# Kernel optimization log

Hardware: AMD Instinct MI355X
Metric: run time of the kernel (lower is better)

The kernel has to match this reference:

```python
import jax, jax.numpy as jnp
import numpy as np

NUM_HEAD = 16
DIM_HEAD = 64
SCALE = DIM_HEAD ** -0.5


def setup_inputs() -> dict:
    key = jax.random.key(0)
    k1, k2, k3 = jax.random.split(key, 3)
    B, N, D = 4, 2048, 1024
    x = jax.random.normal(k1, (B, N, D), dtype=jnp.float32)
    w_qkv = jax.random.normal(k2, (D, 3 * NUM_HEAD * DIM_HEAD), dtype=jnp.float32) * (D ** -0.5)
    w_out = jax.random.normal(k3, (NUM_HEAD * DIM_HEAD, D), dtype=jnp.float32) * ((NUM_HEAD * DIM_HEAD) ** -0.5)
    return {"x": x, "w_qkv": w_qkv, "w_out": w_out}


def reference(x, w_qkv, w_out):
    B, N, D = x.shape
    qkv = x @ w_qkv  # [B, N, 3*H*Dh]
    q, k, v = jnp.split(qkv, 3, axis=-1)
    def heads(t):
        return t.reshape(B, N, NUM_HEAD, DIM_HEAD).transpose(0, 2, 1, 3)  # b h n d
    q, k, v = heads(q), heads(k), heads(v)
    scores = jnp.einsum('bhnd,bhmd->bhnm', q, k) * SCALE
    attn = jax.nn.softmax(scores, axis=-1)
    out = jnp.einsum('bhnm,bhmd->bhnd', attn, v)
    out = out.transpose(0, 2, 1, 3).reshape(B, N, NUM_HEAD * DIM_HEAD)
    return out @ w_out
```

## Files before the change

### kernel.cpp

```cpp
#include <hip/hip_runtime.h>
#include <hip/hip_bf16.h>
#include <stdint.h>


typedef __attribute__((ext_vector_type(8))) __bf16 bf16x8;
typedef __attribute__((ext_vector_type(4))) __bf16 bf16x4;
typedef __attribute__((ext_vector_type(4))) float f32x4;
typedef __attribute__((ext_vector_type(16))) float f32x16;
typedef __attribute__((ext_vector_type(4))) unsigned int u32x4;

#define EXPC 0.18033688011112042f
#define THRR 64.0f

static __device__ __forceinline__ void gload_lds16(const void* g, void* s) {
  __builtin_amdgcn_global_load_lds(
      (__attribute__((address_space(1))) unsigned int*)g,
      (__attribute__((address_space(3))) unsigned int*)s, 16, 0, 0);
}

static __device__ __forceinline__ unsigned pk2(float lo, float hi) {
  unsigned short a = __builtin_bit_cast(unsigned short, (__bf16)lo);
  unsigned short b = __builtin_bit_cast(unsigned short, (__bf16)hi);
  return (unsigned)a | ((unsigned)b << 16);
}

__global__ void k_cvt(const float* __restrict__ src, __bf16* __restrict__ dst, int n4) {
  int i = blockIdx.x * blockDim.x + threadIdx.x;
  if (i >= n4) return;
  float4 v = reinterpret_cast<const float4*>(src)[i];
  bf16x4 o = { (__bf16)v.x, (__bf16)v.y, (__bf16)v.z, (__bf16)v.w };
  *reinterpret_cast<bf16x4*>(dst + (size_t)i * 4) = o;
}

__global__ void k_tcvt(const float* __restrict__ src, __bf16* __restrict__ dst, int W, int Hs) {
  __shared__ float tile[32][33];
  int tx = threadIdx.x, ty = threadIdx.y;
  int x = blockIdx.x * 32 + tx;
  int y0 = blockIdx.y * 32;
  for (int j = ty; j < 32; j += 8) tile[j][tx] = src[(size_t)(y0 + j) * W + x];
  __syncthreads();
  int xo = y0 + tx;
  int yo = blockIdx.x * 32;
  for (int j = ty; j < 32; j += 8) dst[(size_t)(yo + j) * Hs + xo] = (__bf16)tile[tx][j];
}

static __device__ __forceinline__ void gemm_core(
    const __bf16* __restrict__ A, const __bf16* __restrict__ BT, int K,
    int m0, int n0, f32x4 acc[4][4], __bf16* As, __bf16* Bs) {
  const int tid = threadIdx.x;
  const int lane = tid & 63, w = tid >> 6;
  const int fr = lane & 15, fq = lane >> 4;
  const int srow = lane >> 2, scol = (lane & 3) * 8;
  const int wr = (w >> 1) * 64, wc = (w & 1) * 64;
#pragma unroll
  for (int mi = 0; mi < 4; ++mi)
#pragma unroll
    for (int nj = 0; nj < 4; ++nj) acc[mi][nj] = (f32x4){0.f, 0.f, 0.f, 0.f};

  for (int ko = 0; ko < K; ko += 32) {
#pragma unroll
    for (int i = 0; i < 2; ++i) {
      int rb = w * 32 + i * 16;
      gload_lds16(A + (size_t)(m0 + rb + srow) * K + ko + scol, As + rb * 32);
      gload_lds16(BT + (size_t)(n0 + rb + srow) * K + ko + scol, Bs + rb * 32);
    }
    __syncthreads();
    bf16x8 af[4], bfv[4];
#pragma unroll
    for (int mi = 0; mi < 4; ++mi)
      af[mi] = *(const bf16x8*)(As + (wr + mi * 16 + fr) * 32 + fq * 8);
#pragma unroll
    for (int nj = 0; nj < 4; ++nj)
      bfv[nj] = *(const bf16x8*)(Bs + (wc + nj * 16 + fr) * 32 + fq * 8);
#pragma unroll
    for (int mi = 0; mi < 4; ++mi)
#pragma unroll
      for (int nj = 0; nj < 4; ++nj)
        acc[mi][nj] = __builtin_amdgcn_mfma_f32_16x16x32_bf16(af[mi], bfv[nj], acc[mi][nj], 0, 0, 0);
    __syncthreads();
  }
}

__global__ __launch_bounds__(256) void k_gemm_qkv(
    const __bf16* __restrict__ A, const __bf16* __restrict__ BT,
    __bf16* __restrict__ qb, __bf16* __restrict__ kb, __bf16* __restrict__ vb) {
  __shared__ __align__(16) __bf16 As[128 * 32];
  __shared__ __align__(16) __bf16 Bs[128 * 32];
  f32x4 acc[4][4];
  int m0 = blockIdx.x * 128, n0 = blockIdx.y * 128;
  gemm_core(A, BT, 1024, m0, n0, acc, As, Bs);
  const int lane = threadIdx.x & 63, w = threadIdx.x >> 6;
  const int fr = lane & 15, fq = lane >> 4;
  const int wr = (w >> 1) * 64, wc = (w & 1) * 64;
  const int which = n0 >> 10;
#pragma unroll
  for (int mi = 0; mi < 4; ++mi) {
#pragma unroll
    for (int nj = 0; nj < 4; ++nj) {
      int row = m0 + wr + mi * 16 + fq * 4;
      int col = n0 + wc + nj * 16 + fr;
      int rem = col & 1023, h = rem >> 6, d = rem & 63;
      int bb = row >> 11, n = row & 2047;
      int bh = bb * 16 + h;
      if (which == 2) {
        bf16x4 pk = { (__bf16)acc[mi][nj][0], (__bf16)acc[mi][nj][1],
                      (__bf16)acc[mi][nj][2], (__bf16)acc[mi][nj][3] };
        *reinterpret_cast<bf16x4*>(vb + ((size_t)bh * 64 + d) * 2048 + n) = pk;
      } else {
        __bf16* dst = (which == 0) ? qb : kb;
#pragma unroll
        for (int j = 0; j < 4; ++j)
          dst[((size_t)bh * 2048 + (n + j)) * 64 + d] = (__bf16)acc[mi][nj][j];
      }
    }
  }
}

__global__ __launch_bounds__(256) void k_gemm_out(
    const __bf16* __restrict__ A, const __bf16* __restrict__ BT, float* __restrict__ C) {
  __shared__ __align__(16) __bf16 As[128 * 32];
  __shared__ __align__(16) __bf16 Bs[128 * 32];
  f32x4 acc[4][4];
  int m0 = blockIdx.x * 128, n0 = blockIdx.y * 128;
  gemm_core(A, BT, 1024, m0, n0, acc, As, Bs);
  const int lane = threadIdx.x & 63, w = threadIdx.x >> 6;
  const int fr = lane & 15, fq = lane >> 4;
  const int wr = (w >> 1) * 64, wc = (w & 1) * 64;
#pragma unroll
  for (int mi = 0; mi < 4; ++mi)
#pragma unroll
    for (int nj = 0; nj < 4; ++nj)
#pragma unroll
      for (int j = 0; j < 4; ++j)
        C[(size_t)(m0 + wr + mi * 16 + fq * 4 + j) * 1024 + n0 + wc + nj * 16 + fr] =
            acc[mi][nj][j];
}

__global__ __launch_bounds__(256, 3) void k_attn(
    const __bf16* __restrict__ qb, const __bf16* __restrict__ kb,
    const __bf16* __restrict__ vb, __bf16* __restrict__ ao) {
  __shared__ __align__(16) __bf16 Ks[2][64 * 64];
  __shared__ __align__(16) __bf16 Vs[2][64 * 64];
  __shared__ __align__(16) __bf16 Qs[4][32 * 64];
  const int tid = threadIdx.x, lane = tid & 63, wid = tid >> 6;
  const int r31 = lane & 31, hi = lane >> 5;
  const int lsw = (lane & 7) ^ ((lane >> 3) & 3);
  const int bh = blockIdx.x & 63, qblk = blockIdx.x >> 6;
  const __bf16* kbase = kb + (size_t)bh * 2048 * 64;
  const __bf16* vbase = vb + (size_t)bh * 64 * 2048;

  const int nbase = qblk * 128 + wid * 32;

  f32x16 o0, o1;
#pragma unroll
  for (int r = 0; r < 16; ++r) { o0[r] = 0.f; o1[r] = 0.f; }
  float m = -1e30f, lsum = 0.f;

  auto stage = [&](int buf, int j0) {
#pragma unroll
    for (int p2 = 0; p2 < 2; ++p2) {
      int row = p2 * 32 + (tid >> 3);
      int sc = (tid & 7) ^ (row & 7) ^ ((row >> 3) & 3);
      int dst = p2 * 2048 + wid * 512;
      gload_lds16(kbase + (size_t)(j0 + row) * 64 + sc * 8, &Ks[buf][dst]);
      gload_lds16(vbase + (size_t)row * 2048 + j0 + sc * 8, &Vs[buf][dst]);
    }
  };

#pragma unroll
  for (int i = 0; i < 4; ++i) {
    int qr = i * 8 + (lane >> 3);
    int qc = (lane & 7) ^ (qr & 7) ^ ((qr >> 3) & 3);
    gload_lds16(qb + ((size_t)bh * 2048 + nbase + qr) * 64 + qc * 8, &Qs[wid][i * 512]);
  }
  stage(0, 0);
  __syncthreads();

  for (int kt = 0; kt < 32; ++kt) {
    const int cur = kt & 1;
    if (kt < 31) stage(cur ^ 1, (kt + 1) * 64);

    f32x16 sa0, sa1;
#pragma unroll
    for (int r = 0; r < 16; ++r) { sa0[r] = 0.f; sa1[r] = 0.f; }
    __builtin_amdgcn_s_setprio(1);
#pragma unroll
    for (int dd = 0; dd < 4; ++dd) {
      bf16x8 qv = *(const bf16x8*)(&Qs[wid][r31 * 64 + (((dd * 2 + hi) ^ lsw) << 3)]);
      bf16x8 k0 = *(const bf16x8*)(&Ks[cur][r31 * 64 + (((dd * 2 + hi) ^ lsw) << 3)]);
      bf16x8 k1 = *(const bf16x8*)(&Ks[cur][(32 + r31) * 64 + (((dd * 2 + hi) ^ lsw) << 3)]);
      sa0 = __builtin_amdgcn_mfma_f32_32x32x16_bf16(k0, qv, sa0, 0, 0, 0);
      sa1 = __builtin_amdgcn_mfma_f32_32x32x16_bf16(k1, qv, sa1, 0, 0, 0);
    }
    __builtin_amdgcn_s_setprio(0);

    float mx[8];
#pragma unroll
    for (int r = 0; r < 8; ++r)
      mx[r] = fmaxf(fmaxf(fmaxf(sa0[2 * r], sa0[2 * r + 1]), sa1[2 * r]), sa1[2 * r + 1]);
#pragma unroll
    for (int s = 4; s > 0; s >>= 1)
#pragma unroll
      for (int r = 0; r < s; ++r) mx[r] = fmaxf(mx[r], mx[r + s]);
    float pmax = fmaxf(mx[0], __shfl_xor(mx[0], 32, 64));

    if (!__all(pmax - m <= THRR)) {
      float mn = fmaxf(m, pmax);
      float corr = __builtin_amdgcn_exp2f((m - mn) * EXPC);
      m = mn;
      lsum *= corr;
#pragma unroll
      for (int r = 0; r < 16; ++r) {
        int qrow = (r & 3) + 8 * (r >> 2) + 4 * hi;
        float cr = __shfl(corr, qrow, 64);
        o0[r] *= cr; o1[r] *= cr;
      }
    }

    const float mneg = -m * EXPC;
    float rs0 = 0.f, rs1 = 0.f, rs2 = 0.f, rs3 = 0.f;
    unsigned pw0[8], pw1[8];
#pragma unroll
    for (int r = 0; r < 8; ++r) {
      float e0 = __builtin_amdgcn_exp2f(fmaf(sa0[2 * r], EXPC, mneg));
      float e1 = __builtin_amdgcn_exp2f(fmaf(sa0[2 * r + 1], EXPC, mneg));
      float e2 = __builtin_amdgcn_exp2f(fmaf(sa1[2 * r], EXPC, mneg));
      float e3 = __builtin_amdgcn_exp2f(fmaf(sa1[2 * r + 1], EXPC, mneg));
      rs0 += e0; rs1 += e1; rs2 += e2; rs3 += e3;
      pw0[r] = pk2(e0, e1);
      pw1[r] = pk2(e2, e3);
    }
    lsum += (rs0 + rs1) + (rs2 + rs3);

    __builtin_amdgcn_s_setprio(1);
#define PVSTEP(W0, W1, W2, W3, KK) do {                                              \
      unsigned a0 = (W0), a1 = (W1), b0 = (W2), b1 = (W3);                           \
      asm("v_permlane32_swap_b32 %0, %1" : "+v"(a0), "+v"(b0));                      \
      asm("v_permlane32_swap_b32 %0, %1" : "+v"(a1), "+v"(b1));                      \
      u32x4 fw = {a0, a1, b0, b1};                                                   \
      bf16x8 pa = __builtin_bit_cast(bf16x8, fw);                                    \
      bf16x8 v0 = *(const bf16x8*)(&Vs[cur][r31 * 64 + ((((KK)*2 + hi) ^ lsw) << 3)]); \
      bf16x8 v1 = *(const bf16x8*)(&Vs[cur][(32 + r31) * 64 + ((((KK)*2 + hi) ^ lsw) << 3)]); \
      o0 = __builtin_amdgcn_mfma_f32_32x32x16_bf16(pa, v0, o0, 0, 0, 0);             \
      o1 = __builtin_amdgcn_mfma_f32_32x32x16_bf16(pa, v1, o1, 0, 0, 0);             \
    } while (0)
    PVSTEP(pw0[0], pw0[1], pw0[2], pw0[3], 0);
    PVSTEP(pw0[4], pw0[5], pw0[6], pw0[7], 1);
    PVSTEP(pw1[0], pw1[1], pw1[2], pw1[3], 2);
    PVSTEP(pw1[4], pw1[5], pw1[6], pw1[7], 3);
#undef PVSTEP
    __builtin_amdgcn_s_setprio(0);

    __syncthreads();
  }

  lsum += __shfl_xor(lsum, 32, 64);
  float inv = 1.0f / lsum;
  const int b = bh >> 4, h = bh & 15;
  __bf16* abase = ao + ((size_t)b * 2048 + nbase) * 1024 + h * 64 + r31;
#pragma unroll
  for (int r = 0; r < 16; ++r) {
    int qrow = (r & 3) + 8 * (r >> 2) + 4 * hi;
    float ir = __shfl(inv, qrow, 64);
    abase[(size_t)qrow * 1024] = (__bf16)(o0[r] * ir);
    abase[(size_t)qrow * 1024 + 32] = (__bf16)(o1[r] * ir);
  }
}

extern "C" void kernel_launch(void* const* d_in, const int* in_sizes, int n_in,
                              void* d_out, int out_size, void* d_ws, size_t ws_size,
                              hipStream_t stream) {
  (void)in_sizes; (void)n_in; (void)out_size; (void)ws_size;
  const float* x = (const float*)d_in[0];
  const float* w_qkv = (const float*)d_in[1];
  const float* w_out = (const float*)d_in[2];
  float* out = (float*)d_out;

  char* p = (char*)d_ws;
  __bf16* xb    = (__bf16*)p; p += (size_t)8192 * 1024 * 2;
  __bf16* wqkvT = (__bf16*)p; p += (size_t)3072 * 1024 * 2;
  __bf16* woutT = (__bf16*)p; p += (size_t)1024 * 1024 * 2;
  __bf16* qb    = (__bf16*)p; p += (size_t)64 * 2048 * 64 * 2;
  __bf16* kb    = (__bf16*)p; p += (size_t)64 * 2048 * 64 * 2;
  __bf16* vb    = (__bf16*)p; p += (size_t)64 * 64 * 2048 * 2;
  __bf16* ao    = (__bf16*)p; p += (size_t)8192 * 1024 * 2;

  k_cvt<<<8192, 256, 0, stream>>>(x, xb, 2097152);
  k_tcvt<<<dim3(96, 32), dim3(32, 8), 0, stream>>>(w_qkv, wqkvT, 3072, 1024);
  k_tcvt<<<dim3(32, 32), dim3(32, 8), 0, stream>>>(w_out, woutT, 1024, 1024);
  k_gemm_qkv<<<dim3(64, 24), 256, 0, stream>>>(xb, wqkvT, qb, kb, vb);
  k_attn<<<dim3(1024), dim3(256), 0, stream>>>(qb, kb, vb, ao);
  k_gemm_out<<<dim3(64, 8), 256, 0, stream>>>(ao, woutT, out);
}
```

Measured before the change: 215.8 us.

## Load K/V fragments directly from global memory instead of LDS double-buffering

The attention kernel drops the shared-memory double-buffered K/V staging and the per-iteration block barrier. Each wave now reads its MFMA K and V operands straight from global memory (relying on L1/L2 for reuse across the four waves), and occupancy is raised to 4 blocks per SM. It also swaps the software bf16 packing for the v_cvt_pk_bf16_f32 instruction and shortens the row-sum accumulation. This removes LDS traffic and synchronisation, at the risk of exposing global-load latency with no explicit prefetch and of redundant cache reads across waves.

```diff
diff --git a/kernel.cpp b/kernel.cpp
--- a/kernel.cpp
+++ b/kernel.cpp
@@ -16,12 +16,6 @@
   __builtin_amdgcn_global_load_lds(
       (__attribute__((address_space(1))) unsigned int*)g,
       (__attribute__((address_space(3))) unsigned int*)s, 16, 0, 0);
-}
-
-static __device__ __forceinline__ unsigned pk2(float lo, float hi) {
-  unsigned short a = __builtin_bit_cast(unsigned short, (__bf16)lo);
-  unsigned short b = __builtin_bit_cast(unsigned short, (__bf16)hi);
-  return (unsigned)a | ((unsigned)b << 16);
 }
 
 __global__ void k_cvt(const float* __restrict__ src, __bf16* __restrict__ dst, int n4) {
@@ -136,36 +130,15 @@
             acc[mi][nj][j];
 }
 
-__global__ __launch_bounds__(256, 3) void k_attn(
+__global__ __launch_bounds__(256, 4) void k_attn(
     const __bf16* __restrict__ qb, const __bf16* __restrict__ kb,
     const __bf16* __restrict__ vb, __bf16* __restrict__ ao) {
-  __shared__ __align__(16) __bf16 Ks[2][64 * 64];
-  __shared__ __align__(16) __bf16 Vs[2][64 * 64];
   __shared__ __align__(16) __bf16 Qs[4][32 * 64];
   const int tid = threadIdx.x, lane = tid & 63, wid = tid >> 6;
   const int r31 = lane & 31, hi = lane >> 5;
   const int lsw = (lane & 7) ^ ((lane >> 3) & 3);
   const int bh = blockIdx.x & 63, qblk = blockIdx.x >> 6;
-  const __bf16* kbase = kb + (size_t)bh * 2048 * 64;
-  const __bf16* vbase = vb + (size_t)bh * 64 * 2048;
-
   const int nbase = qblk * 128 + wid * 32;
-
-  f32x16 o0, o1;
-#pragma unroll
-  for (int r = 0; r < 16; ++r) { o0[r] = 0.f; o1[r] = 0.f; }
-  float m = -1e30f, lsum = 0.f;
-
-  auto stage = [&](int buf, int j0) {
-#pragma unroll
-    for (int p2 = 0; p2 < 2; ++p2) {
-      int row = p2 * 32 + (tid >> 3);
-      int sc = (tid & 7) ^ (row & 7) ^ ((row >> 3) & 3);
-      int dst = p2 * 2048 + wid * 512;
-      gload_lds16(kbase + (size_t)(j0 + row) * 64 + sc * 8, &Ks[buf][dst]);
-      gload_lds16(vbase + (size_t)row * 2048 + j0 + sc * 8, &Vs[buf][dst]);
-    }
-  };
 
 #pragma unroll
   for (int i = 0; i < 4; ++i) {
@@ -173,12 +146,19 @@
     int qc = (lane & 7) ^ (qr & 7) ^ ((qr >> 3) & 3);
     gload_lds16(qb + ((size_t)bh * 2048 + nbase + qr) * 64 + qc * 8, &Qs[wid][i * 512]);
   }
-  stage(0, 0);
-  __syncthreads();
+  asm volatile("s_waitcnt vmcnt(0)" ::: "memory");
+  __builtin_amdgcn_sched_barrier(0);
+
+  const __bf16* kp = kb + (size_t)bh * 2048 * 64 + r31 * 64 + hi * 8;
+  const __bf16* vp = vb + (size_t)bh * 64 * 2048 + r31 * 2048 + hi * 8;
+
+  f32x16 o0, o1;
+#pragma unroll
+  for (int r = 0; r < 16; ++r) { o0[r] = 0.f; o1[r] = 0.f; }
+  float m = -1e30f, lsum = 0.f;
 
   for (int kt = 0; kt < 32; ++kt) {
-    const int cur = kt & 1;
-    if (kt < 31) stage(cur ^ 1, (kt + 1) * 64);
+    const int j0 = kt * 64;
 
     f32x16 sa0, sa1;
 #pragma unroll
@@ -187,8 +167,8 @@
 #pragma unroll
     for (int dd = 0; dd < 4; ++dd) {
       bf16x8 qv = *(const bf16x8*)(&Qs[wid][r31 * 64 + (((dd * 2 + hi) ^ lsw) << 3)]);
-      bf16x8 k0 = *(const bf16x8*)(&Ks[cur][r31 * 64 + (((dd * 2 + hi) ^ lsw) << 3)]);
-      bf16x8 k1 = *(const bf16x8*)(&Ks[cur][(32 + r31) * 64 + (((dd * 2 + hi) ^ lsw) << 3)]);
+      bf16x8 k0 = *(const bf16x8*)(kp + (size_t)j0 * 64 + dd * 16);
+      bf16x8 k1 = *(const bf16x8*)(kp + (size_t)(j0 + 32) * 64 + dd * 16);
       sa0 = __builtin_amdgcn_mfma_f32_32x32x16_bf16(k0, qv, sa0, 0, 0, 0);
       sa1 = __builtin_amdgcn_mfma_f32_32x32x16_bf16(k1, qv, sa1, 0, 0, 0);
     }
@@ -218,7 +198,7 @@
     }
 
     const float mneg = -m * EXPC;
-    float rs0 = 0.f, rs1 = 0.f, rs2 = 0.f, rs3 = 0.f;
+    float rs0 = 0.f, rs1 = 0.f;
     unsigned pw0[8], pw1[8];
 #pragma unroll
     for (int r = 0; r < 8; ++r) {
@@ -226,11 +206,11 @@
       float e1 = __builtin_amdgcn_exp2f(fmaf(sa0[2 * r + 1], EXPC, mneg));
       float e2 = __builtin_amdgcn_exp2f(fmaf(sa1[2 * r], EXPC, mneg));
       float e3 = __builtin_amdgcn_exp2f(fmaf(sa1[2 * r + 1], EXPC, mneg));
-      rs0 += e0; rs1 += e1; rs2 += e2; rs3 += e3;
-      pw0[r] = pk2(e0, e1);
-      pw1[r] = pk2(e2, e3);
-    }
-    lsum += (rs0 + rs1) + (rs2 + rs3);
+      rs0 += e0 + e1; rs1 += e2 + e3;
+      asm("v_cvt_pk_bf16_f32 %0, %1, %2" : "=v"(pw0[r]) : "v"(e0), "v"(e1));
+      asm("v_cvt_pk_bf16_f32 %0, %1, %2" : "=v"(pw1[r]) : "v"(e2), "v"(e3));
+    }
+    lsum += rs0 + rs1;
 
     __builtin_amdgcn_s_setprio(1);
 #define PVSTEP(W0, W1, W2, W3, KK) do {                                              \
@@ -239,8 +219,8 @@
       asm("v_permlane32_swap_b32 %0, %1" : "+v"(a1), "+v"(b1));                      \
       u32x4 fw = {a0, a1, b0, b1};                                                   \
       bf16x8 pa = __builtin_bit_cast(bf16x8, fw);                                    \
-      bf16x8 v0 = *(const bf16x8*)(&Vs[cur][r31 * 64 + ((((KK)*2 + hi) ^ lsw) << 3)]); \
-      bf16x8 v1 = *(const bf16x8*)(&Vs[cur][(32 + r31) * 64 + ((((KK)*2 + hi) ^ lsw) << 3)]); \
+      bf16x8 v0 = *(const bf16x8*)(vp + j0 + (KK) * 16);                             \
+      bf16x8 v1 = *(const bf16x8*)(vp + (size_t)32 * 2048 + j0 + (KK) * 16);         \
       o0 = __builtin_amdgcn_mfma_f32_32x32x16_bf16(pa, v0, o0, 0, 0, 0);             \
       o1 = __builtin_amdgcn_mfma_f32_32x32x16_bf16(pa, v1, o1, 0, 0, 0);             \
     } while (0)
@@ -250,8 +230,6 @@
     PVSTEP(pw1[4], pw1[5], pw1[6], pw1[7], 3);
 #undef PVSTEP
     __builtin_amdgcn_s_setprio(0);
-
-    __syncthreads();
   }
 
   lsum += __shfl_xor(lsum, 32, 64);
```

Result: slower. 336.4 us (+55.9%).

## Keep Q in registers, split KV tile into halves, raise attention occupancy

Applied to the files above, without the earlier changes.

The attention kernel now loads Q fragments straight from global memory into registers instead of staging them through LDS. Each 64-key tile is processed as two 32-key halves with separate softmax updates, which halves the live score registers. Launch bounds move from 3 to 4 blocks per CU, and the bf16 packing uses the v_cvt_pk_bf16_f32 instruction. The aim is higher occupancy and less LDS traffic, at the cost of more online-softmax max/rescale steps and shorter MFMA chains per half.

```diff
diff --git a/kernel.cpp b/kernel.cpp
--- a/kernel.cpp
+++ b/kernel.cpp
@@ -16,12 +16,6 @@
   __builtin_amdgcn_global_load_lds(
       (__attribute__((address_space(1))) unsigned int*)g,
       (__attribute__((address_space(3))) unsigned int*)s, 16, 0, 0);
-}
-
-static __device__ __forceinline__ unsigned pk2(float lo, float hi) {
-  unsigned short a = __builtin_bit_cast(unsigned short, (__bf16)lo);
-  unsigned short b = __builtin_bit_cast(unsigned short, (__bf16)hi);
-  return (unsigned)a | ((unsigned)b << 16);
 }
 
 __global__ void k_cvt(const float* __restrict__ src, __bf16* __restrict__ dst, int n4) {
@@ -136,12 +130,11 @@
             acc[mi][nj][j];
 }
 
-__global__ __launch_bounds__(256, 3) void k_attn(
+__global__ __launch_bounds__(256, 4) void k_attn(
     const __bf16* __restrict__ qb, const __bf16* __restrict__ kb,
     const __bf16* __restrict__ vb, __bf16* __restrict__ ao) {
   __shared__ __align__(16) __bf16 Ks[2][64 * 64];
   __shared__ __align__(16) __bf16 Vs[2][64 * 64];
-  __shared__ __align__(16) __bf16 Qs[4][32 * 64];
   const int tid = threadIdx.x, lane = tid & 63, wid = tid >> 6;
   const int r31 = lane & 31, hi = lane >> 5;
   const int lsw = (lane & 7) ^ ((lane >> 3) & 3);
@@ -150,6 +143,11 @@
   const __bf16* vbase = vb + (size_t)bh * 64 * 2048;
 
   const int nbase = qblk * 128 + wid * 32;
+  const __bf16* qptr = qb + ((size_t)bh * 2048 + nbase + r31) * 64;
+  bf16x8 qf[4];
+#pragma unroll
+  for (int dd = 0; dd < 4; ++dd)
+    qf[dd] = *(const bf16x8*)(qptr + dd * 16 + hi * 8);
 
   f32x16 o0, o1;
 #pragma unroll
@@ -167,12 +165,6 @@
     }
   };
 
-#pragma unroll
-  for (int i = 0; i < 4; ++i) {
-    int qr = i * 8 + (lane >> 3);
-    int qc = (lane & 7) ^ (qr & 7) ^ ((qr >> 3) & 3);
-    gload_lds16(qb + ((size_t)bh * 2048 + nbase + qr) * 64 + qc * 8, &Qs[wid][i * 512]);
-  }
   stage(0, 0);
   __syncthreads();
 
@@ -180,76 +172,72 @@
     const int cur = kt & 1;
     if (kt < 31) stage(cur ^ 1, (kt + 1) * 64);
 
-    f32x16 sa0, sa1;
-#pragma unroll
-    for (int r = 0; r < 16; ++r) { sa0[r] = 0.f; sa1[r] = 0.f; }
-    __builtin_amdgcn_s_setprio(1);
-#pragma unroll
-    for (int dd = 0; dd < 4; ++dd) {
-      bf16x8 qv = *(const bf16x8*)(&Qs[wid][r31 * 64 + (((dd * 2 + hi) ^ lsw) << 3)]);
-      bf16x8 k0 = *(const bf16x8*)(&Ks[cur][r31 * 64 + (((dd * 2 + hi) ^ lsw) << 3)]);
-      bf16x8 k1 = *(const bf16x8*)(&Ks[cur][(32 + r31) * 64 + (((dd * 2 + hi) ^ lsw) << 3)]);
-      sa0 = __builtin_amdgcn_mfma_f32_32x32x16_bf16(k0, qv, sa0, 0, 0, 0);
-      sa1 = __builtin_amdgcn_mfma_f32_32x32x16_bf16(k1, qv, sa1, 0, 0, 0);
-    }
-    __builtin_amdgcn_s_setprio(0);
-
-    float mx[8];
-#pragma unroll
-    for (int r = 0; r < 8; ++r)
-      mx[r] = fmaxf(fmaxf(fmaxf(sa0[2 * r], sa0[2 * r + 1]), sa1[2 * r]), sa1[2 * r + 1]);
-#pragma unroll
-    for (int s = 4; s > 0; s >>= 1)
-#pragma unroll
-      for (int r = 0; r < s; ++r) mx[r] = fmaxf(mx[r], mx[r + s]);
-    float pmax = fmaxf(mx[0], __shfl_xor(mx[0], 32, 64));
-
-    if (!__all(pmax - m <= THRR)) {
-      float mn = fmaxf(m, pmax);
-      float corr = __builtin_amdgcn_exp2f((m - mn) * EXPC);
-      m = mn;
-      lsum *= corr;
-#pragma unroll
-      for (int r = 0; r < 16; ++r) {
-        int qrow = (r & 3) + 8 * (r >> 2) + 4 * hi;
-        float cr = __shfl(corr, qrow, 64);
-        o0[r] *= cr; o1[r] *= cr;
-      }
-    }
-
-    const float mneg = -m * EXPC;
-    float rs0 = 0.f, rs1 = 0.f, rs2 = 0.f, rs3 = 0.f;
-    unsigned pw0[8], pw1[8];
-#pragma unroll
-    for (int r = 0; r < 8; ++r) {
-      float e0 = __builtin_amdgcn_exp2f(fmaf(sa0[2 * r], EXPC, mneg));
-      float e1 = __builtin_amdgcn_exp2f(fmaf(sa0[2 * r + 1], EXPC, mneg));
-      float e2 = __builtin_amdgcn_exp2f(fmaf(sa1[2 * r], EXPC, mneg));
-      float e3 = __builtin_amdgcn_exp2f(fmaf(sa1[2 * r + 1], EXPC, mneg));
-      rs0 += e0; rs1 += e1; rs2 += e2; rs3 += e3;
-      pw0[r] = pk2(e0, e1);
-      pw1[r] = pk2(e2, e3);
-    }
-    lsum += (rs0 + rs1) + (rs2 + rs3);
-
-    __builtin_amdgcn_s_setprio(1);
+#pragma unroll
+    for (int h2 = 0; h2 < 2; ++h2) {
+      const int kro = h2 * 32;
+
+      f32x16 sa;
+#pragma unroll
+      for (int r = 0; r < 16; ++r) sa[r] = 0.f;
+      __builtin_amdgcn_s_setprio(1);
+#pragma unroll
+      for (int dd = 0; dd < 4; ++dd) {
+        bf16x8 kf = *(const bf16x8*)(&Ks[cur][(kro + r31) * 64 + (((dd * 2 + hi) ^ lsw) << 3)]);
+        sa = __builtin_amdgcn_mfma_f32_32x32x16_bf16(kf, qf[dd], sa, 0, 0, 0);
+      }
+      __builtin_amdgcn_s_setprio(0);
+
+      float mx[8];
+#pragma unroll
+      for (int r = 0; r < 8; ++r) mx[r] = fmaxf(sa[2 * r], sa[2 * r + 1]);
+#pragma unroll
+      for (int s = 4; s > 0; s >>= 1)
+#pragma unroll
+        for (int r = 0; r < s; ++r) mx[r] = fmaxf(mx[r], mx[r + s]);
+      float pmax = fmaxf(mx[0], __shfl_xor(mx[0], 32, 64));
+
+      if (!__all(pmax - m <= THRR)) {
+        float mn = fmaxf(m, pmax);
+        float corr = __builtin_amdgcn_exp2f((m - mn) * EXPC);
+        m = mn;
+        lsum *= corr;
+#pragma unroll
+        for (int r = 0; r < 16; ++r) {
+          int qrow = (r & 3) + 8 * (r >> 2) + 4 * hi;
+          float cr = __shfl(corr, qrow, 64);
+          o0[r] *= cr; o1[r] *= cr;
+        }
+      }
+
+      const float mneg = -m * EXPC;
+      float rs0 = 0.f, rs1 = 0.f;
+      unsigned pw[8];
+#pragma unroll
+      for (int r = 0; r < 8; ++r) {
+        float e0 = __builtin_amdgcn_exp2f(fmaf(sa[2 * r], EXPC, mneg));
+        float e1 = __builtin_amdgcn_exp2f(fmaf(sa[2 * r + 1], EXPC, mneg));
+        rs0 += e0; rs1 += e1;
+        asm("v_cvt_pk_bf16_f32 %0, %1, %2" : "=v"(pw[r]) : "v"(e0), "v"(e1));
+      }
+      lsum += rs0 + rs1;
+
+      __builtin_amdgcn_s_setprio(1);
 #define PVSTEP(W0, W1, W2, W3, KK) do {                                              \
-      unsigned a0 = (W0), a1 = (W1), b0 = (W2), b1 = (W3);                           \
-      asm("v_permlane32_swap_b32 %0, %1" : "+v"(a0), "+v"(b0));                      \
-      asm("v_permlane32_swap_b32 %0, %1" : "+v"(a1), "+v"(b1));                      \
-      u32x4 fw = {a0, a1, b0, b1};                                                   \
-      bf16x8 pa = __builtin_bit_cast(bf16x8, fw);                                    \
-      bf16x8 v0 = *(const bf16x8*)(&Vs[cur][r31 * 64 + ((((KK)*2 + hi) ^ lsw) << 3)]); \
-      bf16x8 v1 = *(const bf16x8*)(&Vs[cur][(32 + r31) * 64 + ((((KK)*2 + hi) ^ lsw) << 3)]); \
-      o0 = __builtin_amdgcn_mfma_f32_32x32x16_bf16(pa, v0, o0, 0, 0, 0);             \
-      o1 = __builtin_amdgcn_mfma_f32_32x32x16_bf16(pa, v1, o1, 0, 0, 0);             \
-    } while (0)
-    PVSTEP(pw0[0], pw0[1], pw0[2], pw0[3], 0);
-    PVSTEP(pw0[4], pw0[5], pw0[6], pw0[7], 1);
-    PVSTEP(pw1[0], pw1[1], pw1[2], pw1[3], 2);
-    PVSTEP(pw1[4], pw1[5], pw1[6], pw1[7], 3);
+        unsigned a0 = (W0), a1 = (W1), b0 = (W2), b1 = (W3);                         \
+        asm("v_permlane32_swap_b32 %0, %1" : "+v"(a0), "+v"(b0));                    \
+        asm("v_permlane32_swap_b32 %0, %1" : "+v"(a1), "+v"(b1));                    \
+        u32x4 fw = {a0, a1, b0, b1};                                                 \
+        bf16x8 pa = __builtin_bit_cast(bf16x8, fw);                                  \
+        bf16x8 v0 = *(const bf16x8*)(&Vs[cur][r31 * 64 + ((((KK) * 2 + hi) ^ lsw) << 3)]); \
+        bf16x8 v1 = *(const bf16x8*)(&Vs[cur][(32 + r31) * 64 + ((((KK) * 2 + hi) ^ lsw) << 3)]); \
+        o0 = __builtin_amdgcn_mfma_f32_32x32x16_bf16(pa, v0, o0, 0, 0, 0);           \
+        o1 = __builtin_amdgcn_mfma_f32_32x32x16_bf16(pa, v1, o1, 0, 0, 0);           \
+      } while (0)
+      PVSTEP(pw[0], pw[1], pw[2], pw[3], 2 * h2);
+      PVSTEP(pw[4], pw[5], pw[6], pw[7], 2 * h2 + 1);
 #undef PVSTEP
-    __builtin_amdgcn_s_setprio(0);
+      __builtin_amdgcn_s_setprio(0);
+    }
 
     __syncthreads();
   }
```

New measurement: 205.4 us. 4.8% less time.
